# Optimization experiments

Measured on AMD Instinct MI355X. Metric: run time of the kernel, lower is better.

## Reference

```python
import jax, jax.numpy as jnp
import numpy as np
from jax import lax

STRIDES = (8, 16, 32, 64, 128)
NUM_CONVS = 4
IN_CH = 256
NUM_CLASSES = 80
NUM_REG = 4  # reg head outputs NUM_REG + 1 channels (centerness first)
SIZES = [(128, 128), (64, 64), (32, 32), (16, 16), (8, 8)]
BATCH = 4


def _conv(x, w):
    # x: (N,C,H,W), w: (O,I,kh,kw), stride 1, SAME padding
    return lax.conv_general_dilated(x, w, (1, 1), 'SAME',
                                    dimension_numbers=('NCHW', 'OIHW', 'NCHW'))


def _head(x, conv_w, bn_scale, bn_bias, final_w, final_b):
    # Shared decoder: NUM_CONVS x (3x3 conv -> BN(eval, folded to scale/bias) -> ReLU),
    # then 1x1 pointwise conv with bias.
    for i in range(NUM_CONVS):
        x = _conv(x, conv_w[i])
        x = x * bn_scale[i][None, :, None, None] + bn_bias[i][None, :, None, None]
        x = jnp.maximum(x, 0.0)
    return _conv(x, final_w) + final_b[None, :, None, None]


def setup_inputs() -> dict:
    key = jax.random.key(0)
    ks = jax.random.split(key, 16)
    inp = {}
    for i, (h, w) in enumerate(SIZES):
        inp[f'fpn{i}'] = jax.random.normal(ks[i], (BATCH, IN_CH, h, w), dtype=jnp.float32)
    wstd = 0.02
    inp['cls_conv_w'] = jax.random.normal(ks[5], (NUM_CONVS, IN_CH, IN_CH, 3, 3), dtype=jnp.float32) * wstd
    inp['cls_bn_scale'] = jnp.ones((NUM_CONVS, IN_CH), dtype=jnp.float32) + 0.1 * jax.random.normal(ks[6], (NUM_CONVS, IN_CH), dtype=jnp.float32)
    inp['cls_bn_bias'] = 0.1 * jax.random.normal(ks[7], (NUM_CONVS, IN_CH), dtype=jnp.float32)
    inp['cls_final_w'] = jax.random.normal(ks[8], (NUM_CLASSES, IN_CH, 1, 1), dtype=jnp.float32) * wstd
    # prior-prob bias init: -log((1-0.01)/0.01)
    inp['cls_final_b'] = jnp.full((NUM_CLASSES,), -float(np.log(99.0)), dtype=jnp.float32)
    inp['reg_conv_w'] = jax.random.normal(ks[9], (NUM_CONVS, IN_CH, IN_CH, 3, 3), dtype=jnp.float32) * wstd
    inp['reg_bn_scale'] = jnp.ones((NUM_CONVS, IN_CH), dtype=jnp.float32) + 0.1 * jax.random.normal(ks[10], (NUM_CONVS, IN_CH), dtype=jnp.float32)
    inp['reg_bn_bias'] = 0.1 * jax.random.normal(ks[11], (NUM_CONVS, IN_CH), dtype=jnp.float32)
    inp['reg_final_w'] = jax.random.normal(ks[12], (NUM_REG + 1, IN_CH, 1, 1), dtype=jnp.float32) * wstd
    inp['reg_final_b'] = jax.random.normal(ks[13], (NUM_REG + 1,), dtype=jnp.float32) * 0.1
    return inp


def reference(fpn0, fpn1, fpn2, fpn3, fpn4,
              cls_conv_w, cls_bn_scale, cls_bn_bias, cls_final_w, cls_final_b,
              reg_conv_w, reg_bn_scale, reg_bn_bias, reg_final_w, reg_final_b):
    fpn = (fpn0, fpn1, fpn2, fpn3, fpn4)
    cls = tuple(_head(x, cls_conv_w, cls_bn_scale, cls_bn_bias, cls_final_w, cls_final_b) for x in fpn)
    raw = tuple(_head(x, reg_conv_w, reg_bn_scale, reg_bn_bias, reg_final_w, reg_final_b) for x in fpn)
    centerness = tuple(r[:, 0:1, :, :] for r in raw)
    reg = tuple(jnp.maximum(r[:, 1:, :, :] * float(s), 0.0) for r, s in zip(raw, STRIDES))
    # flatten (cls_list, reg_list, centerness_list) into one tuple of 15 arrays
    return cls + reg + centerness
```

## Files before the change

kernel.cpp:

```cpp
#include <hip/hip_runtime.h>

typedef __attribute__((ext_vector_type(8))) short short8;
typedef __attribute__((ext_vector_type(4))) float f32x4;

#define ACT_P 23384064ul
#define WSTEP 589824

__device__ unsigned short g_actC[ACT_P];
__device__ unsigned short g_actA0[ACT_P];
__device__ unsigned short g_actB0[ACT_P];
__device__ unsigned short g_actA1[ACT_P];
__device__ unsigned short g_actB1[ACT_P];
__device__ unsigned short g_wc[4 * WSTEP];
__device__ unsigned short g_wr[4 * WSTEP];
__device__ unsigned short g_w1c[80 * 256];

__constant__ int      C_W[5]    = {128, 64, 32, 16, 8};
__constant__ int      C_WP[5]   = {130, 66, 34, 18, 10};
__constant__ int      C_HWP[5]  = {16900, 4356, 1156, 324, 100};
__constant__ int      C_LW[5]   = {7, 6, 5, 4, 3};
__constant__ int      C_LXT[5]  = {4, 3, 2, 1, 0};
__constant__ int      C_PREF[5] = {0, 128, 160, 168, 170};
__constant__ int      C_HW[5]   = {16384, 4096, 1024, 256, 64};
__constant__ unsigned C_LOFFP[5]= {0u, 17305600u, 21766144u, 22949888u, 23281664u};
__constant__ unsigned C_CLSO[5] = {0u, 5242880u, 6553600u, 6881280u, 6963200u};
__constant__ unsigned C_REGO[5] = {6983680u, 7245824u, 7311360u, 7327744u, 7331840u};
__constant__ unsigned C_CENTO[5]= {7332864u, 7398400u, 7414784u, 7418880u, 7419904u};
__constant__ float    C_STRF[5] = {8.f, 16.f, 32.f, 64.f, 128.f};

static __device__ __forceinline__ unsigned short f2bf(float f) {
    unsigned u = __float_as_uint(f);
    unsigned r = (u + 0x7FFFu + ((u >> 16) & 1u)) >> 16;
    return (unsigned short)r;
}
static __device__ __forceinline__ float bf2f(unsigned short b) {
    return __uint_as_float(((unsigned)b) << 16);
}

#define GLOAD0(dst, ptr) \
    asm volatile("global_load_dwordx4 %0, %1, off" : "=v"(dst) : "v"(ptr))
#define GLOAD_OFF(dst, ptr, imm) \
    asm volatile("global_load_dwordx4 %0, %1, off offset:" #imm : "=v"(dst) : "v"(ptr))

static __device__ __forceinline__ void vmwait(int n) {
    switch (n) {
    case 0:  asm volatile("s_waitcnt vmcnt(0)"  ::: "memory"); break;
    case 1:  asm volatile("s_waitcnt vmcnt(1)"  ::: "memory"); break;
    case 2:  asm volatile("s_waitcnt vmcnt(2)"  ::: "memory"); break;
    case 3:  asm volatile("s_waitcnt vmcnt(3)"  ::: "memory"); break;
    case 4:  asm volatile("s_waitcnt vmcnt(4)"  ::: "memory"); break;
    case 5:  asm volatile("s_waitcnt vmcnt(5)"  ::: "memory"); break;
    case 6:  asm volatile("s_waitcnt vmcnt(6)"  ::: "memory"); break;
    case 7:  asm volatile("s_waitcnt vmcnt(7)"  ::: "memory"); break;
    case 8:  asm volatile("s_waitcnt vmcnt(8)"  ::: "memory"); break;
    default: asm volatile("s_waitcnt vmcnt(9)"  ::: "memory"); break;
    }
    __builtin_amdgcn_sched_barrier(0);
}

__global__ __launch_bounds__(256) void cvt_w3(
    const float* __restrict__ wc, const float* __restrict__ wr,
    unsigned short* __restrict__ oc, unsigned short* __restrict__ orr)
{
    const int co = blockIdx.x, sm = blockIdx.y, head = blockIdx.z;
    const int step = sm / 9, tap = sm - step * 9;
    const int ci = threadIdx.x;
    const float* w = head ? wr : wc;
    unsigned short* o = head ? orr : oc;
    o[(((size_t)sm * 32 + (ci >> 3)) * 256 + co) * 8 + (ci & 7)] =
        f2bf(w[(((size_t)step * 256 + co) * 256 + ci) * 9 + tap]);
}

__global__ __launch_bounds__(256) void cvt_w1(
    const float* __restrict__ w, unsigned short* __restrict__ o)
{
    for (int idx = threadIdx.x; idx < 80 * 256; idx += 256)
        o[idx] = f2bf(w[idx]);
}

__global__ __launch_bounds__(256) void zero_halo(
    unsigned short* c, unsigned short* a0, unsigned short* b0,
    unsigned short* a1, unsigned short* b1)
{
    unsigned short* bufs[5] = {c, a0, b0, a1, b1};
    const int bid = blockIdx.x;
    const int buf = bid / 20, r = bid - buf * 20, lvl = r >> 2, n = r & 3;
    const int Wp = C_WP[lvl], Hp = Wp;
    unsigned short* base = bufs[buf] + C_LOFFP[lvl] + (size_t)n * C_HWP[lvl] * 256;
    const int hc = 2 * Wp + 2 * (Hp - 2);
    uint4 z; z.x = z.y = z.z = z.w = 0u;
    for (int idx = threadIdx.x; idx < hc * 32; idx += 256) {
        int pos = idx >> 5, q = idx & 31;
        int row, col;
        if (pos < 2 * Wp) { row = (pos >= Wp) ? (Hp - 1) : 0; col = (pos >= Wp) ? pos - Wp : pos; }
        else { int rem = pos - 2 * Wp; row = 1 + (rem >> 1); col = (rem & 1) ? (Wp - 1) : 0; }
        *(uint4*)(base + ((size_t)(row * Wp + col) << 8) + q * 8) = z;
    }
}

__global__ __launch_bounds__(256) void cvt_in(
    const float* __restrict__ f0, const float* __restrict__ f1,
    const float* __restrict__ f2, const float* __restrict__ f3,
    const float* __restrict__ f4, unsigned short* __restrict__ dstC)
{
    const int lvl = blockIdx.y, n = blockIdx.z;
    const int HW = C_HW[lvl];
    const int p0 = blockIdx.x * 64;
    if (p0 >= HW) return;
    const int W = C_W[lvl], lw = C_LW[lvl], Wp = C_WP[lvl];
    const float* fp[5] = {f0, f1, f2, f3, f4};
    const float* src = fp[lvl] + (size_t)n * 256 * HW;
    unsigned short* dst = dstC + C_LOFFP[lvl] + (size_t)n * C_HWP[lvl] * 256;
    const int tid = threadIdx.x;
    __shared__ float ts[64][65];

    for (int cc = 0; cc < 256; cc += 64) {
        for (int idx = tid; idx < 64 * 64; idx += 256) {
            int ci = idx >> 6, p = idx & 63;
            ts[ci][p] = src[(size_t)(cc + ci) * HW + p0 + p];
        }
        __syncthreads();
        for (int idx = tid; idx < 64 * 64; idx += 256) {
            int p = idx >> 6, ci = idx & 63;
            int gp = p0 + p, y = gp >> lw, x = gp & (W - 1);
            dst[(size_t)((y + 1) * Wp + x + 1) * 256 + cc + ci] = f2bf(ts[ci][p]);
        }
        __syncthreads();
    }
}

__global__ __launch_bounds__(512, 2) void conv3x3_mfma(
    const unsigned short* __restrict__ src0, const unsigned short* __restrict__ src1,
    unsigned short* __restrict__ dst0, unsigned short* __restrict__ dst1,
    const unsigned short* __restrict__ wt0, const unsigned short* __restrict__ wt1,
    const float* __restrict__ sc0, const float* __restrict__ bi0,
    const float* __restrict__ sc1, const float* __restrict__ bi1)
{
    int tc = blockIdx.x;
    const int lvl = (tc >= 128) + (tc >= 160) + (tc >= 168) + (tc >= 170);
    tc -= C_PREF[lvl];
    const int head = blockIdx.z >> 2, n = blockIdx.z & 3;

    const int W = C_W[lvl], H = W, Wp = C_WP[lvl];
    const int lxt = C_LXT[lvl];
    const int tx = tc & ((1 << lxt) - 1), ty = tc >> lxt;
    const int x0 = tx * 8, y0 = ty * 16;

    const unsigned short* src = head ? src1 : src0;
    unsigned short*       dst = head ? dst1 : dst0;
    const unsigned short* wt  = head ? wt1 : wt0;
    const float* sc = head ? sc1 : sc0;
    const float* bi = head ? bi1 : bi0;
    const size_t actOff = (size_t)C_LOFFP[lvl] + (size_t)n * C_HWP[lvl] * 256;
    src += actOff; dst += actOff;

    const int tid = threadIdx.x;
    const int lane = tid & 63, wid = tid >> 6;
    const int l16 = lane & 15, quad = lane >> 4;
    const int cow = wid * 32;

    __shared__ unsigned short B_s[32 * 10 * 19 * 8];
    char* Bb = (char*)B_s;

    int goff[6], ldso[6];
#pragma unroll
    for (int it = 0; it < 6; it++) {
        int slot = tid + it * 512;
        if (slot > 2879) slot = 2879;
        int g = slot & 15, p = slot >> 4;
        int y = (p * 205) >> 11;
        int x = p - y * 10;
        int gyp = y0 + y; if (gyp > Wp - 1) gyp = Wp - 1;
        goff[it] = (((gyp * Wp) + x0 + x) << 8) + g * 8;
        ldso[it] = ((g * 10 + x) * 19 + y) * 16;
    }

    f32x4 acc[2][8];
#pragma unroll
    for (int mf = 0; mf < 2; mf++)
#pragma unroll
        for (int nf = 0; nf < 8; nf++) acc[mf][nf] = (f32x4){0.f, 0.f, 0.f, 0.f};

    {
        uint4 tv[6];
#pragma unroll
        for (int it = 0; it < 6; it++) tv[it] = *(const uint4*)(src + goff[it]);
#pragma unroll
        for (int it = 0; it < 6; it++) *(uint4*)(Bb + ldso[it]) = tv[it];
    }
    __syncthreads();

#pragma unroll
    for (int ph = 0; ph < 2; ph++) {
        if (ph == 1) {
            uint4 tv[6];
#pragma unroll
            for (int it = 0; it < 6; it++) tv[it] = *(const uint4*)(src + goff[it] + 128);
#pragma unroll
            for (int it = 0; it < 6; it++) *(uint4*)(Bb + ldso[it] + 48640) = tv[it];
            __syncthreads();
        }

        short8 Af[4][2];
        short8 Bf[2][10];

        auto wBase = [&](int T) -> const unsigned short* {
            const int c4 = T / 9, tap = T - 9 * c4;
            const int c32 = ph * 4 + c4;
            return wt + (((tap * 32 + c32 * 4 + quad) * 256) + cow + l16) * 8;
        };
        auto issueA = [&](int T, short8* dA) {
            const unsigned short* p = wBase(T);
            GLOAD0(dA[0], p);
            GLOAD_OFF(dA[1], p, 256);
        };
        auto loadB = [&](int g, short8* dB) {
            const int c4 = g / 3, kh = g - 3 * c4;
            const int c32 = ph * 4 + c4;
#pragma unroll
            for (int j = 0; j < 10; j++)
                dB[j] = *(const short8*)(Bb +
                    (((c32 * 4 + quad) * 10 + j) * 19 + l16 + kh) * 16);
        };

#pragma unroll
        for (int t = 0; t < 3; t++) issueA(t, Af[t]);
        loadB(0, Bf[0]);

#pragma unroll
        for (int T = 0; T < 36; T++) {
            const int g = T / 3, kw = T - g * 3;
            if (T + 3 < 36) issueA(T + 3, Af[(T + 3) & 3]);
            if (kw == 0 && g + 1 < 12) loadB(g + 1, Bf[(g + 1) & 1]);
            const int lead = (T + 3 < 36) ? 3 : (35 - T);
            const short8* Ac = Af[T & 3];
            const short8* Bc = Bf[g & 1];
#pragma unroll
            for (int mf = 0; mf < 2; mf++) {
                vmwait(2 * lead + (1 - mf));
#pragma unroll
                for (int nf = 0; nf < 8; nf++)
                    acc[mf][nf] = __builtin_amdgcn_mfma_f32_16x16x32_bf16(
                        Ac[mf], Bc[nf + kw], acc[mf][nf], 0, 0, 0);
            }
        }
    }

    const int gy = y0 + l16;
    if (gy < H) {
#pragma unroll
        for (int mf = 0; mf < 2; mf++) {
            const int co4 = cow + mf * 16 + quad * 4;
            const f32x4 s4 = *(const f32x4*)(sc + co4);
            const f32x4 b4 = *(const f32x4*)(bi + co4);
#pragma unroll
            for (int nf = 0; nf < 8; nf++) {
                const int gx = x0 + nf;
                f32x4 v = acc[mf][nf];
                ushort4 o;
                o.x = f2bf(fmaxf(v[0] * s4[0] + b4[0], 0.f));
                o.y = f2bf(fmaxf(v[1] * s4[1] + b4[1], 0.f));
                o.z = f2bf(fmaxf(v[2] * s4[2] + b4[2], 0.f));
                o.w = f2bf(fmaxf(v[3] * s4[3] + b4[3], 0.f));
                *(ushort4*)(dst + ((size_t)((gy + 1) * Wp + gx + 1) * 256 + co4)) = o;
            }
        }
    }
}

__global__ __launch_bounds__(256) void final_cls(
    const unsigned short* __restrict__ act, const unsigned short* __restrict__ w,
    const float* __restrict__ bias, float* __restrict__ out)
{
    const int lvl = blockIdx.y, n = blockIdx.z;
    const int HW = C_HW[lvl];
    const int p0 = blockIdx.x * 128;
    if (p0 >= HW) return;
    const int W = C_W[lvl], lw = C_LW[lvl], Wp = C_WP[lvl];

    const int tid = threadIdx.x;
    const int lane = tid & 63, wid = tid >> 6;
    const int l16 = lane & 15, quad = lane >> 4;

    const unsigned short* a = act + C_LOFFP[lvl] + (size_t)n * C_HWP[lvl] * 256;

    int px[2]; size_t aoff[2];
#pragma unroll
    for (int j = 0; j < 2; j++) {
        px[j] = p0 + wid * 32 + j * 16 + l16;
        int lpx = px[j] < HW ? px[j] : 0;
        int y = lpx >> lw, x = lpx & (W - 1);
        aoff[j] = (size_t)((y + 1) * Wp + x + 1) * 256;
    }

    f32x4 acc[5][2];
#pragma unroll
    for (int mf = 0; mf < 5; mf++) { acc[mf][0] = (f32x4){0,0,0,0}; acc[mf][1] = (f32x4){0,0,0,0}; }

    for (int cc = 0; cc < 256; cc += 32) {
        short8 b0 = *(const short8*)(a + aoff[0] + cc + quad * 8);
        short8 b1 = *(const short8*)(a + aoff[1] + cc + quad * 8);
#pragma unroll
        for (int mf = 0; mf < 5; mf++) {
            short8 av = *(const short8*)(w + (mf * 16 + l16) * 256 + cc + quad * 8);
            acc[mf][0] = __builtin_amdgcn_mfma_f32_16x16x32_bf16(av, b0, acc[mf][0], 0, 0, 0);
            acc[mf][1] = __builtin_amdgcn_mfma_f32_16x16x32_bf16(av, b1, acc[mf][1], 0, 0, 0);
        }
    }

    float* ob = out + C_CLSO[lvl] + (size_t)n * 80 * HW;
#pragma unroll
    for (int mf = 0; mf < 5; mf++) {
        const int co0 = mf * 16 + quad * 4;
#pragma unroll
        for (int j = 0; j < 2; j++) {
            if (px[j] < HW) {
#pragma unroll
                for (int r = 0; r < 4; r++)
                    ob[(size_t)(co0 + r) * HW + px[j]] = acc[mf][j][r] + bias[co0 + r];
            }
        }
    }
}

__global__ __launch_bounds__(256) void final_reg(
    const unsigned short* __restrict__ act, const float* __restrict__ w,
    const float* __restrict__ bias, float* __restrict__ out)
{
    const int lvl = blockIdx.y, n = blockIdx.z;
    const int HW = C_HW[lvl];
    const int W = C_W[lvl], lw = C_LW[lvl], Wp = C_WP[lvl];
    const int tid = threadIdx.x;

    __shared__ float ws[5 * 256];
    for (int idx = tid; idx < 5 * 256; idx += 256) ws[idx] = w[idx];
    __syncthreads();

    const int px = blockIdx.x * 256 + tid;
    if (px >= HW) return;

    const int y = px >> lw, x = px & (W - 1);
    const unsigned short* a = act + C_LOFFP[lvl] + (size_t)n * C_HWP[lvl] * 256
                            + (size_t)((y + 1) * Wp + x + 1) * 256;
    float acc[5] = {0.f, 0.f, 0.f, 0.f, 0.f};

    for (int ci = 0; ci < 256; ci += 8) {
        ushort4 u0 = *(const ushort4*)(a + ci);
        ushort4 u1 = *(const ushort4*)(a + ci + 4);
        float xv[8] = {bf2f(u0.x), bf2f(u0.y), bf2f(u0.z), bf2f(u0.w),
                       bf2f(u1.x), bf2f(u1.y), bf2f(u1.z), bf2f(u1.w)};
#pragma unroll
        for (int j = 0; j < 5; j++) {
            const float* wj = &ws[j * 256 + ci];
#pragma unroll
            for (int k = 0; k < 8; k++) acc[j] = fmaf(xv[k], wj[k], acc[j]);
        }
    }

    const float strf = C_STRF[lvl];
    out[C_CENTO[lvl] + (size_t)n * HW + px] = acc[0] + bias[0];
    float* rb = out + C_REGO[lvl] + (size_t)n * 4 * HW;
#pragma unroll
    for (int j = 0; j < 4; j++)
        rb[(size_t)j * HW + px] = fmaxf((acc[j + 1] + bias[j + 1]) * strf, 0.f);
}

extern "C" void kernel_launch(void* const* d_in, const int* in_sizes, int n_in,
                              void* d_out, int out_size, void* d_ws, size_t ws_size,
                              hipStream_t stream)
{
    const float* cls_w  = (const float*)d_in[5];
    const float* cls_s  = (const float*)d_in[6];
    const float* cls_b  = (const float*)d_in[7];
    const float* cls_fw = (const float*)d_in[8];
    const float* cls_fb = (const float*)d_in[9];
    const float* reg_w  = (const float*)d_in[10];
    const float* reg_s  = (const float*)d_in[11];
    const float* reg_b  = (const float*)d_in[12];
    const float* reg_fw = (const float*)d_in[13];
    const float* reg_fb = (const float*)d_in[14];
    float* out = (float*)d_out;

    unsigned short *actC, *actA0, *actB0, *actA1, *actB1, *wc, *wr, *w1c;
    hipGetSymbolAddress((void**)&actC,  HIP_SYMBOL(g_actC));
    hipGetSymbolAddress((void**)&actA0, HIP_SYMBOL(g_actA0));
    hipGetSymbolAddress((void**)&actB0, HIP_SYMBOL(g_actB0));
    hipGetSymbolAddress((void**)&actA1, HIP_SYMBOL(g_actA1));
    hipGetSymbolAddress((void**)&actB1, HIP_SYMBOL(g_actB1));
    hipGetSymbolAddress((void**)&wc,    HIP_SYMBOL(g_wc));
    hipGetSymbolAddress((void**)&wr,    HIP_SYMBOL(g_wr));
    hipGetSymbolAddress((void**)&w1c,   HIP_SYMBOL(g_w1c));

    cvt_w3<<<dim3(256, 36, 2), 256, 0, stream>>>(cls_w, reg_w, wc, wr);
    cvt_w1<<<1, 256, 0, stream>>>(cls_fw, w1c);
    zero_halo<<<100, 256, 0, stream>>>(actC, actA0, actB0, actA1, actB1);
    cvt_in<<<dim3(256, 5, 4), 256, 0, stream>>>(
        (const float*)d_in[0], (const float*)d_in[1], (const float*)d_in[2],
        (const float*)d_in[3], (const float*)d_in[4], actC);

    unsigned short* srcs[4][2] = {{actC, actC}, {actA0, actA1}, {actB0, actB1}, {actA0, actA1}};
    unsigned short* dsts[4][2] = {{actA0, actA1}, {actB0, actB1}, {actA0, actA1}, {actB0, actB1}};
    for (int s = 0; s < 4; s++) {
        conv3x3_mfma<<<dim3(171, 1, 8), 512, 0, stream>>>(
            srcs[s][0], srcs[s][1], dsts[s][0], dsts[s][1],
            wc + (size_t)s * WSTEP, wr + (size_t)s * WSTEP,
            cls_s + s * 256, cls_b + s * 256, reg_s + s * 256, reg_b + s * 256);
    }

    final_cls<<<dim3(128, 5, 4), 256, 0, stream>>>(actB0, w1c, cls_fb, out);
    final_reg<<<dim3(64, 5, 4), 256, 0, stream>>>(actB1, reg_fw, reg_fb, out);
}
```

Baseline: 953.2 us.

## Switch 3x3 conv inner loop to 32x32x16 bf16 MFMA tiles

Rewrites the conv kernel's MMA loop to use 32x32x16 MFMA instructions, each covering 32 output channels by 32 pixels (2 columns by 16 rows), instead of 16x16x32 instructions. This reduces the number of MFMA issues and LDS B-fragment loads per K-step: 4 B loads per step instead of 10 per group. It also simplifies the weight prefetch to one load per step with a shallower vmcnt wait. The accumulator layout and the epilogue indexing are remapped to match. Risks include different LDS bank-conflict patterns and less reuse of B across kw shifts, since each kw tap now reloads B.

```diff
diff --git a/kernel.cpp b/kernel.cpp
--- a/kernel.cpp
+++ b/kernel.cpp
@@ -2,6 +2,7 @@
 
 typedef __attribute__((ext_vector_type(8))) short short8;
 typedef __attribute__((ext_vector_type(4))) float f32x4;
+typedef __attribute__((ext_vector_type(16))) float f32x16;
 
 #define ACT_P 23384064ul
 #define WSTEP 589824
@@ -39,8 +40,6 @@
 
 #define GLOAD0(dst, ptr) \
     asm volatile("global_load_dwordx4 %0, %1, off" : "=v"(dst) : "v"(ptr))
-#define GLOAD_OFF(dst, ptr, imm) \
-    asm volatile("global_load_dwordx4 %0, %1, off offset:" #imm : "=v"(dst) : "v"(ptr))
 
 static __device__ __forceinline__ void vmwait(int n) {
     switch (n) {
@@ -49,11 +48,7 @@
     case 2:  asm volatile("s_waitcnt vmcnt(2)"  ::: "memory"); break;
     case 3:  asm volatile("s_waitcnt vmcnt(3)"  ::: "memory"); break;
     case 4:  asm volatile("s_waitcnt vmcnt(4)"  ::: "memory"); break;
-    case 5:  asm volatile("s_waitcnt vmcnt(5)"  ::: "memory"); break;
-    case 6:  asm volatile("s_waitcnt vmcnt(6)"  ::: "memory"); break;
-    case 7:  asm volatile("s_waitcnt vmcnt(7)"  ::: "memory"); break;
-    case 8:  asm volatile("s_waitcnt vmcnt(8)"  ::: "memory"); break;
-    default: asm volatile("s_waitcnt vmcnt(9)"  ::: "memory"); break;
+    default: asm volatile("s_waitcnt vmcnt(5)"  ::: "memory"); break;
     }
     __builtin_amdgcn_sched_barrier(0);
 }
@@ -156,7 +151,10 @@
 
     const int tid = threadIdx.x;
     const int lane = tid & 63, wid = tid >> 6;
-    const int l16 = lane & 15, quad = lane >> 4;
+    const int l16 = lane & 15;
+    const int l31 = lane & 31;
+    const int xh1 = (lane >> 4) & 1;
+    const int gh  = lane >> 5;
     const int cow = wid * 32;
 
     __shared__ unsigned short B_s[32 * 10 * 19 * 8];
@@ -175,11 +173,11 @@
         ldso[it] = ((g * 10 + x) * 19 + y) * 16;
     }
 
-    f32x4 acc[2][8];
-#pragma unroll
-    for (int mf = 0; mf < 2; mf++)
-#pragma unroll
-        for (int nf = 0; nf < 8; nf++) acc[mf][nf] = (f32x4){0.f, 0.f, 0.f, 0.f};
+    f32x16 acc[4];
+#pragma unroll
+    for (int ng = 0; ng < 4; ng++)
+#pragma unroll
+        for (int r = 0; r < 16; r++) acc[ng][r] = 0.f;
 
     {
         uint4 tv[6];
@@ -201,68 +199,61 @@
             __syncthreads();
         }
 
-        short8 Af[4][2];
-        short8 Bf[2][10];
-
-        auto wBase = [&](int T) -> const unsigned short* {
-            const int c4 = T / 9, tap = T - 9 * c4;
-            const int c32 = ph * 4 + c4;
-            return wt + (((tap * 32 + c32 * 4 + quad) * 256) + cow + l16) * 8;
+        short8 Af[4];
+        short8 Bf[2][4];
+
+        const unsigned short* wbase =
+            wt + (((size_t)(ph * 16 + gh) * 256) + cow + l31) * 8;
+        char* bbase = Bb + ph * 48640 + ((gh * 10 + xh1) * 19 + l16) * 16;
+
+        auto issueA = [&](int S) {
+            const int tap = S >> 3, ks = S & 7;
+            GLOAD0(Af[S & 3], wbase + tap * 65536 + ks * 4096);
         };
-        auto issueA = [&](int T, short8* dA) {
-            const unsigned short* p = wBase(T);
-            GLOAD0(dA[0], p);
-            GLOAD_OFF(dA[1], p, 256);
+        auto loadB = [&](int S, short8* dB) {
+            const int tap = S >> 3, ks = S & 7;
+            const int kh = tap / 3, kw = tap - 3 * kh;
+#pragma unroll
+            for (int ng = 0; ng < 4; ng++)
+                dB[ng] = *(const short8*)(bbase +
+                    ks * 6080 + (ng * 2 + kw) * 304 + kh * 16);
         };
-        auto loadB = [&](int g, short8* dB) {
-            const int c4 = g / 3, kh = g - 3 * c4;
-            const int c32 = ph * 4 + c4;
-#pragma unroll
-            for (int j = 0; j < 10; j++)
-                dB[j] = *(const short8*)(Bb +
-                    (((c32 * 4 + quad) * 10 + j) * 19 + l16 + kh) * 16);
-        };
-
-#pragma unroll
-        for (int t = 0; t < 3; t++) issueA(t, Af[t]);
+
+#pragma unroll
+        for (int t = 0; t < 3; t++) issueA(t);
         loadB(0, Bf[0]);
 
 #pragma unroll
-        for (int T = 0; T < 36; T++) {
-            const int g = T / 3, kw = T - g * 3;
-            if (T + 3 < 36) issueA(T + 3, Af[(T + 3) & 3]);
-            if (kw == 0 && g + 1 < 12) loadB(g + 1, Bf[(g + 1) & 1]);
-            const int lead = (T + 3 < 36) ? 3 : (35 - T);
-            const short8* Ac = Af[T & 3];
-            const short8* Bc = Bf[g & 1];
-#pragma unroll
-            for (int mf = 0; mf < 2; mf++) {
-                vmwait(2 * lead + (1 - mf));
-#pragma unroll
-                for (int nf = 0; nf < 8; nf++)
-                    acc[mf][nf] = __builtin_amdgcn_mfma_f32_16x16x32_bf16(
-                        Ac[mf], Bc[nf + kw], acc[mf][nf], 0, 0, 0);
-            }
-        }
-    }
-
-    const int gy = y0 + l16;
-    if (gy < H) {
-#pragma unroll
-        for (int mf = 0; mf < 2; mf++) {
-            const int co4 = cow + mf * 16 + quad * 4;
-            const f32x4 s4 = *(const f32x4*)(sc + co4);
-            const f32x4 b4 = *(const f32x4*)(bi + co4);
-#pragma unroll
-            for (int nf = 0; nf < 8; nf++) {
-                const int gx = x0 + nf;
-                f32x4 v = acc[mf][nf];
+        for (int S = 0; S < 72; S++) {
+            if (S + 3 < 72) issueA(S + 3);
+            if (S + 1 < 72) loadB(S + 1, Bf[(S + 1) & 1]);
+            vmwait((S + 3 < 72) ? 3 : (71 - S));
+            const short8 a = Af[S & 3];
+            const short8* Bc = Bf[S & 1];
+#pragma unroll
+            for (int ng = 0; ng < 4; ng++)
+                acc[ng] = __builtin_amdgcn_mfma_f32_32x32x16_bf16(
+                    a, Bc[ng], acc[ng], 0, 0, 0);
+        }
+    }
+
+    const int oy = y0 + l16;
+    if (oy < H) {
+#pragma unroll
+        for (int ng = 0; ng < 4; ng++) {
+            const int ox = x0 + ng * 2 + xh1;
+            unsigned short* drow = dst + ((size_t)((oy + 1) * Wp + ox + 1) * 256);
+#pragma unroll
+            for (int q = 0; q < 4; q++) {
+                const int co4 = cow + gh * 4 + q * 8;
+                const f32x4 s4 = *(const f32x4*)(sc + co4);
+                const f32x4 b4 = *(const f32x4*)(bi + co4);
                 ushort4 o;
-                o.x = f2bf(fmaxf(v[0] * s4[0] + b4[0], 0.f));
-                o.y = f2bf(fmaxf(v[1] * s4[1] + b4[1], 0.f));
-                o.z = f2bf(fmaxf(v[2] * s4[2] + b4[2], 0.f));
-                o.w = f2bf(fmaxf(v[3] * s4[3] + b4[3], 0.f));
-                *(ushort4*)(dst + ((size_t)((gy + 1) * Wp + gx + 1) * 256 + co4)) = o;
+                o.x = f2bf(fmaxf(acc[ng][q * 4 + 0] * s4[0] + b4[0], 0.f));
+                o.y = f2bf(fmaxf(acc[ng][q * 4 + 1] * s4[1] + b4[1], 0.f));
+                o.z = f2bf(fmaxf(acc[ng][q * 4 + 2] * s4[2] + b4[2], 0.f));
+                o.w = f2bf(fmaxf(acc[ng][q * 4 + 3] * s4[3] + b4[3], 0.f));
+                *(ushort4*)(drow + co4) = o;
             }
         }
     }
```

After: 1.105 ms. 1.16x slower.
